# Kernel optimization log

Hardware: AMD Instinct MI355X
Metric: run time of the kernel (lower is better)

## Reference

```python
import jax, jax.numpy as jnp
import numpy as np

H = 768          # low-res grid side
S = 3            # scale_factor -> output is (H*S, H*S)
HID = 32         # hidden_channels
N = H * H


def _grid_edges(h):
    """8-neighbor directed edge list, same as create_graph's python loop."""
    idx = np.arange(h * h, dtype=np.int32).reshape(h, h)
    srcs, dsts = [], []
    for di in (-1, 0, 1):
        for dj in (-1, 0, 1):
            if di == 0 and dj == 0:
                continue
            rs = slice(max(0, -di), h - max(0, di))
            cs = slice(max(0, -dj), h - max(0, dj))
            rd = slice(max(0, di), h - max(0, -di))
            cd = slice(max(0, dj), h - max(0, -dj))
            srcs.append(idx[rs, cs].ravel())
            dsts.append(idx[rd, cd].ravel())
    return np.stack([np.concatenate(srcs), np.concatenate(dsts)])


def setup_inputs() -> dict:
    key = jax.random.key(0)
    ks = jax.random.split(key, 4)
    edge_index = jnp.asarray(_grid_edges(H))  # [2, E] int32
    x = jax.random.normal(ks[0], (N, 3), dtype=jnp.float32)
    W1 = jax.random.normal(ks[1], (3, HID), dtype=jnp.float32) * (1.0 / np.sqrt(3))
    W2 = jax.random.normal(ks[2], (HID, HID), dtype=jnp.float32) * (1.0 / np.sqrt(HID))
    W3 = jax.random.normal(ks[3], (HID, S * S), dtype=jnp.float32) * (1.0 / np.sqrt(HID))
    return {
        "x": x, "edge_index": edge_index,
        "W1": W1, "b1": jnp.zeros((HID,), jnp.float32),
        "W2": W2, "b2": jnp.zeros((HID,), jnp.float32),
        "W3": W3, "b3": jnp.zeros((S * S,), jnp.float32),
    }


def _gcn_layer(h, W, b, src, dst, norm_e, self_norm, n):
    # GCNConv: x' = D^-1/2 (A + I) D^-1/2 (x W) + b
    h = h @ W
    msg = h[src] * norm_e[:, None]                        # gather + normalize
    agg = jax.ops.segment_sum(msg, dst, num_segments=n)    # scatter-add
    return agg + h * self_norm[:, None] + b                # self-loop + bias


def reference(x, edge_index, W1, b1, W2, b2, W3, b3):
    n = x.shape[0]
    src, dst = edge_index[0], edge_index[1]
    # degrees with self-loops (PyG gcn_norm: deg on target col, +1 self loop)
    deg = jax.ops.segment_sum(jnp.ones(src.shape, jnp.float32), dst, num_segments=n) + 1.0
    dinv = jax.lax.rsqrt(deg)
    norm_e = dinv[src] * dinv[dst]
    self_norm = dinv * dinv

    h = jax.nn.relu(_gcn_layer(x, W1, b1, src, dst, norm_e, self_norm, n))
    h = jax.nn.relu(_gcn_layer(h, W2, b2, src, dst, norm_e, self_norm, n))
    h = _gcn_layer(h, W3, b3, src, dst, norm_e, self_norm, n)

    # pixel-shuffle reshape: [N, S*S] -> [1, H*S, H*S]
    out = h.reshape(1, H, H, S, S).transpose(0, 1, 3, 2, 4).reshape(1, H * S, H * S)
    return out
```

## Files before the change

### kernel.cpp

```cpp
#include <hip/hip_runtime.h>


constexpr int HH = 768, SS = 3;
constexpr int TI = 12, TJ = 24;
constexpr int NBJ = 32;
constexpr int NT = 512;

constexpr int G0C = 30;  constexpr int N0  = 540;
constexpr int S0C = 28;  constexpr int NS0 = 448;
constexpr int R3C = 26;  constexpr int NS1 = 364;
constexpr int NS1P = 368;
constexpr int ON  = 288;

constexpr int G1O = 0;
constexpr int D3O = 7168;
constexpr int SMEMF = 7536;

constexpr int TB0 = 0;
constexpr int TB1 = 1472;
constexpr int TB2 = 2944;
constexpr int OUT0 = 3328;
constexpr int OUT1 = 4480;
constexpr int OUT2 = 5632;

#define SWZ(row) ((((row) >> 1) & 3) << 2)

typedef _Float16 f16x8 __attribute__((ext_vector_type(8)));
typedef float    f32x4 __attribute__((ext_vector_type(4)));
using h2 = decltype(__builtin_amdgcn_cvt_pkrtz(0.f, 0.f));

#define PK(a, b)  __builtin_amdgcn_cvt_pkrtz((a), (b))
#define BC2(u)    __builtin_bit_cast(h2, (u))
#define BCU(x)    __builtin_bit_cast(uint32_t, (x))
#define MFMA16(a, b, c) __builtin_amdgcn_mfma_f32_16x16x32_f16((a), (b), (c), 0, 0, 0)

__device__ __forceinline__ float dinv_of(int gi, int gj) {
    int e = (1 + (gi > 0) + (gi < HH - 1)) * (1 + (gj > 0) + (gj < HH - 1));
    return e == 9 ? 0.33333334f : (e == 6 ? 0.40824829f : 0.5f);
}
__device__ __forceinline__ void add4(float4& a, const float4 v) {
    a.x += v.x; a.y += v.y; a.z += v.z; a.w += v.w;
}
#define FMA4G(acc, s, wp) { const float4 _w = *(const float4*)(wp); \
    acc.x += (s) * _w.x; acc.y += (s) * _w.y; acc.z += (s) * _w.z; acc.w += (s) * _w.w; }

__global__ __launch_bounds__(NT, 8) void gnn_fused(
    const float* __restrict__ x,
    const float* __restrict__ W1, const float* __restrict__ b1,
    const float* __restrict__ W2, const float* __restrict__ b2,
    const float* __restrict__ W3, const float* __restrict__ b3,
    float* __restrict__ out)
{
    __shared__ __align__(16) float smem[SMEMF];
    const int tid = threadIdx.x;
    const int lane = tid & 63, wid = tid >> 6;
    const int lr = lane & 15, lg = lane >> 4;
    const int bi = blockIdx.x / NBJ;
    const int bj = blockIdx.x % NBJ;
    const int oi = bi * TI, oj = bj * TJ;

    for (int n = tid; n < N0; n += NT) {
        int li = n / G0C, lj = n - li * G0C;
        int gi = oi - 3 + li, gj = oj - 3 + lj;
        float4 v = {0.f, 0.f, 0.f, 0.f};
        if ((unsigned)gi < HH && (unsigned)gj < HH) {
            float d = dinv_of(gi, gj);
            const float* xp = x + 3 * ((size_t)gi * HH + gj);
            v.x = d * xp[0]; v.y = d * xp[1]; v.z = d * xp[2];
        }
        *(float4*)&smem[G1O + n * 4] = v;
    }
    if (tid < NS1P) {
        float v = 0.f;
        if (tid < NS1) {
            int li = tid / R3C, lj = tid - li * R3C;
            int gi = oi - 1 + li, gj = oj - 1 + lj;
            if ((unsigned)gi < HH && (unsigned)gj < HH) v = dinv_of(gi, gj);
        }
        smem[D3O + tid] = v;
    }
    __syncthreads();

    float4 s0a = {0,0,0,0};
    float d2a = 0.f;
    if (tid < NS0) {
        int li = tid / S0C, lj = tid - li * S0C;
        int base = li * G0C + lj;
        #pragma unroll
        for (int di = 0; di < 3; ++di)
            #pragma unroll
            for (int dj = 0; dj < 3; ++dj)
                add4(s0a, *(const float4*)&smem[G1O + (base + di * G0C + dj) * 4]);
        int gi = oi - 2 + li, gj = oj - 2 + lj;
        if ((unsigned)gi < HH && (unsigned)gj < HH) d2a = dinv_of(gi, gj);
    }
    const int nA0 = wid * 16 + lr;
    const int nA1 = (wid + 8) * 16 + lr;
    const int nA2 = (wid + 16) * 16 + lr;
    const int fb0 = (nA0 / R3C) * S0C + (nA0 % R3C);
    const int fb1 = (nA1 / R3C) * S0C + (nA1 % R3C);
    const int fb2 = (nA2 / R3C) * S0C + (nA2 % R3C);
    __syncthreads();

    uint4 uw20, uw21, uw3;
    {
        const int k0 = 8 * lg;
        uw20.x = BCU(PK(W2[(k0+0)*32 + lr],      W2[(k0+1)*32 + lr]));
        uw20.y = BCU(PK(W2[(k0+2)*32 + lr],      W2[(k0+3)*32 + lr]));
        uw20.z = BCU(PK(W2[(k0+4)*32 + lr],      W2[(k0+5)*32 + lr]));
        uw20.w = BCU(PK(W2[(k0+6)*32 + lr],      W2[(k0+7)*32 + lr]));
        uw21.x = BCU(PK(W2[(k0+0)*32 + 16 + lr], W2[(k0+1)*32 + 16 + lr]));
        uw21.y = BCU(PK(W2[(k0+2)*32 + 16 + lr], W2[(k0+3)*32 + 16 + lr]));
        uw21.z = BCU(PK(W2[(k0+4)*32 + 16 + lr], W2[(k0+5)*32 + 16 + lr]));
        uw21.w = BCU(PK(W2[(k0+6)*32 + 16 + lr], W2[(k0+7)*32 + 16 + lr]));
        float a0w=0.f,b0w=0.f,a1w=0.f,b1w=0.f,a2w=0.f,b2w=0.f,a3w=0.f,b3w=0.f;
        if (lr < 9) {
            a0w = W3[(k0+0)*9 + lr]; b0w = W3[(k0+1)*9 + lr];
            a1w = W3[(k0+2)*9 + lr]; b1w = W3[(k0+3)*9 + lr];
            a2w = W3[(k0+4)*9 + lr]; b2w = W3[(k0+5)*9 + lr];
            a3w = W3[(k0+6)*9 + lr]; b3w = W3[(k0+7)*9 + lr];
        }
        uw3.x = BCU(PK(a0w, b0w)); uw3.y = BCU(PK(a1w, b1w));
        uw3.z = BCU(PK(a2w, b2w)); uw3.w = BCU(PK(a3w, b3w));
    }
    const float b2c0 = b2[lr], b2c1 = b2[16 + lr];

    if (tid < NS0) {
        uint32_t g[16];
        #pragma unroll
        for (int q = 0; q < 8; ++q) {
            float4 a = {0,0,0,0};
            FMA4G(a, s0a.x, W1 + 4 * q)
            FMA4G(a, s0a.y, W1 + 32 + 4 * q)
            FMA4G(a, s0a.z, W1 + 64 + 4 * q)
            const float4 bb = *(const float4*)&b1[4 * q];
            float gx = d2a * fmaxf(d2a * a.x + bb.x, 0.f);
            float gy = d2a * fmaxf(d2a * a.y + bb.y, 0.f);
            float gz = d2a * fmaxf(d2a * a.z + bb.z, 0.f);
            float gw = d2a * fmaxf(d2a * a.w + bb.w, 0.f);
            g[2 * q]     = BCU(PK(gx, gy));
            g[2 * q + 1] = BCU(PK(gz, gw));
        }
        const int sz = SWZ(tid);
        uint4 u;
        u.x = g[0];  u.y = g[1];  u.z = g[2];  u.w = g[3];
        *(uint4*)&smem[G1O + tid * 16 + (0 ^ sz)] = u;
        u.x = g[4];  u.y = g[5];  u.z = g[6];  u.w = g[7];
        *(uint4*)&smem[G1O + tid * 16 + (4 ^ sz)] = u;
        u.x = g[8];  u.y = g[9];  u.z = g[10]; u.w = g[11];
        *(uint4*)&smem[G1O + tid * 16 + (8 ^ sz)] = u;
        u.x = g[12]; u.y = g[13]; u.z = g[14]; u.w = g[15];
        *(uint4*)&smem[G1O + tid * 16 + (12 ^ sz)] = u;
    }
    __syncthreads();

    const f16x8 bw20 = __builtin_bit_cast(f16x8, uw20);
    const f16x8 bw21 = __builtin_bit_cast(f16x8, uw21);
    const f16x8 bw3  = __builtin_bit_cast(f16x8, uw3);

    #define TAP(rr) (*(const uint4*)&smem[G1O + (rr) * 16 + ((4 * lg) ^ SWZ(rr))])
    #define ROWSUM(rr, o0, o1, o2) { \
        const uint4 va = TAP((rr)+(o0)); const uint4 vb = TAP((rr)+(o1)); const uint4 vc = TAP((rr)+(o2)); \
        r0 = (BC2(va.x) + BC2(vb.x)) + BC2(vc.x); \
        r1 = (BC2(va.y) + BC2(vb.y)) + BC2(vc.y); \
        r2 = (BC2(va.z) + BC2(vb.z)) + BC2(vc.z); \
        r3 = (BC2(va.w) + BC2(vb.w)) + BC2(vc.w); }

    #define BS2MM2(fb, cc0, cc1) { \
        h2 r0, r1, r2, r3, s0_, s1_, s2_, s3_; \
        ROWSUM((fb), 0, 1, 2)               s0_ = r0; s1_ = r1; s2_ = r2; s3_ = r3; \
        ROWSUM((fb) + S0C, 0, 1, 2)         s0_ += r0; s1_ += r1; s2_ += r2; s3_ += r3; \
        ROWSUM((fb) + 2 * S0C, 0, 1, 2)     s0_ += r0; s1_ += r1; s2_ += r2; s3_ += r3; \
        uint4 af_; af_.x = BCU(s0_); af_.y = BCU(s1_); af_.z = BCU(s2_); af_.w = BCU(s3_); \
        const f16x8 aa_ = __builtin_bit_cast(f16x8, af_); \
        cc0 = MFMA16(aa_, bw20, cc0); \
        cc1 = MFMA16(aa_, bw21, cc1); }

    f32x4 c00 = {0,0,0,0}, c01 = {0,0,0,0};
    f32x4 c10 = {0,0,0,0}, c11 = {0,0,0,0};
    f32x4 c20 = {0,0,0,0}, c21 = {0,0,0,0};
    BS2MM2(fb0, c00, c01)
    BS2MM2(fb1, c10, c11)
    if (wid < 7) { BS2MM2(fb2, c20, c21) }
    __syncthreads();

    _Float16* hp = (_Float16*)smem;
    #define WRH(rt, cc0, cc1) { \
        const int nb = (rt) * 16 + lg * 4; \
        const float4 dd = *(const float4*)&smem[D3O + nb]; \
        _Pragma("unroll") \
        for (int r = 0; r < 4; ++r) { \
            const float dv = r == 0 ? dd.x : (r == 1 ? dd.y : (r == 2 ? dd.z : dd.w)); \
            const float h0 = dv * fmaxf(dv * cc0[r] + b2c0, 0.f); \
            const float h1 = dv * fmaxf(dv * cc1[r] + b2c1, 0.f); \
            const int row_ = nb + r; \
            const int sz_ = SWZ(row_); \
            hp[2 * (G1O + row_ * 16 + (((lr >> 1)) ^ sz_)) + (lr & 1)] = (_Float16)h0; \
            hp[2 * (G1O + row_ * 16 + ((8 + (lr >> 1)) ^ sz_)) + (lr & 1)] = (_Float16)h1; } }

    WRH(wid, c00, c01)
    WRH(wid + 8, c10, c11)
    if (wid < 7) { WRH(wid + 16, c20, c21) }
    __syncthreads();

    #define AFRAG(rt) __builtin_bit_cast(f16x8, \
        *(const uint4*)&smem[G1O + ((rt) * 16 + lr) * 16 + ((4 * lg) ^ SWZ((rt) * 16 + lr))])
    f16x8 a30 = AFRAG(wid);
    f16x8 a31 = AFRAG(wid + 8);
    f16x8 a32 = a30;
    if (wid < 7) a32 = AFRAG(wid + 16);
    __syncthreads();

    #define MM3TILE(rt, af) { \
        f32x4 tt = {0.f, 0.f, 0.f, 0.f}; \
        tt = MFMA16((af), bw3, tt); \
        const int nb = (rt) * 16 + lg * 4; \
        if (lr < 4) { \
            smem[TB0 + (nb + 0) * 4 + lr] = tt[0]; \
            smem[TB0 + (nb + 1) * 4 + lr] = tt[1]; \
            smem[TB0 + (nb + 2) * 4 + lr] = tt[2]; \
            smem[TB0 + (nb + 3) * 4 + lr] = tt[3]; \
        } else if (lr < 8) { \
            smem[TB1 + (nb + 0) * 4 + lr - 4] = tt[0]; \
            smem[TB1 + (nb + 1) * 4 + lr - 4] = tt[1]; \
            smem[TB1 + (nb + 2) * 4 + lr - 4] = tt[2]; \
            smem[TB1 + (nb + 3) * 4 + lr - 4] = tt[3]; \
        } else if (lr == 8) { \
            smem[TB2 + nb + 0] = tt[0]; \
            smem[TB2 + nb + 1] = tt[1]; \
            smem[TB2 + nb + 2] = tt[2]; \
            smem[TB2 + nb + 3] = tt[3]; } }

    MM3TILE(wid, a30)
    MM3TILE(wid + 8, a31)
    if (wid < 7) { MM3TILE(wid + 16, a32) }
    __syncthreads();

    for (int item = tid; item < 3 * ON; item += NT) {
        int p = item / ON, n = item - p * ON;
        int li = n / TJ, lj = n - li * TJ;
        int src = li * R3C + lj;
        float d = dinv_of(oi + li, oj + lj);
        if (p == 2) {
            float s = 0.f;
            #pragma unroll
            for (int di = 0; di < 3; ++di)
                #pragma unroll
                for (int dj = 0; dj < 3; ++dj)
                    s += smem[TB2 + src + di * R3C + dj];
            smem[OUT2 + n] = d * s + b3[8];
        } else {
            const int tb = p ? TB1 : TB0;
            float4 s = {0.f, 0.f, 0.f, 0.f};
            #pragma unroll
            for (int di = 0; di < 3; ++di)
                #pragma unroll
                for (int dj = 0; dj < 3; ++dj)
                    add4(s, *(const float4*)&smem[tb + (src + di * R3C + dj) * 4]);
            const float4 bb = *(const float4*)&b3[4 * p];
            float4 o;
            o.x = d * s.x + bb.x; o.y = d * s.y + bb.y;
            o.z = d * s.z + bb.z; o.w = d * s.w + bb.w;
            *(float4*)&smem[(p ? OUT1 : OUT0) + n * 4] = o;
        }
    }
    __syncthreads();

    #define ORD(n, c) ((c) < 8 ? smem[((c) < 4 ? OUT0 : OUT1) + (n) * 4 + ((c) & 3)] \
                               : smem[OUT2 + (n)])
    for (int q = tid; q < 36 * 18; q += NT) {
        int rr = q / 18, cc0 = 4 * (q % 18);
        int ii = rr / 3, si = rr - 3 * ii;
        float4 o;
        { int cc = cc0 + 0, jj = cc / 3, sj = cc - 3 * jj; o.x = ORD(ii * TJ + jj, si * 3 + sj); }
        { int cc = cc0 + 1, jj = cc / 3, sj = cc - 3 * jj; o.y = ORD(ii * TJ + jj, si * 3 + sj); }
        { int cc = cc0 + 2, jj = cc / 3, sj = cc - 3 * jj; o.z = ORD(ii * TJ + jj, si * 3 + sj); }
        { int cc = cc0 + 3, jj = cc / 3, sj = cc - 3 * jj; o.w = ORD(ii * TJ + jj, si * 3 + sj); }
        *(float4*)&out[(size_t)(oi * SS + rr) * (HH * SS) + oj * SS + cc0] = o;
    }
}

extern "C" void kernel_launch(void* const* d_in, const int* in_sizes, int n_in,
                              void* d_out, int out_size, void* d_ws, size_t ws_size,
                              hipStream_t stream) {
    const float* x  = (const float*)d_in[0];
    const float* W1 = (const float*)d_in[2];
    const float* b1 = (const float*)d_in[3];
    const float* W2 = (const float*)d_in[4];
    const float* b2 = (const float*)d_in[5];
    const float* W3 = (const float*)d_in[6];
    const float* b3 = (const float*)d_in[7];
    float* out = (float*)d_out;

    gnn_fused<<<dim3(64 * NBJ), dim3(NT), 0, stream>>>(x, W1, b1, W2, b2, W3, b3, out);
}
```

Baseline: 38.38 us.

## Aggregate layer-3 inputs before the W3 MFMA and fuse the normalization epilogue

```diff
diff --git a/kernel.cpp b/kernel.cpp
--- a/kernel.cpp
+++ b/kernel.cpp
@@ -14,16 +14,13 @@
 
 constexpr int G1O = 0;
 constexpr int D3O = 7168;
-constexpr int SMEMF = 7536;
-
-constexpr int TB0 = 0;
-constexpr int TB1 = 1472;
-constexpr int TB2 = 2944;
-constexpr int OUT0 = 3328;
-constexpr int OUT1 = 4480;
-constexpr int OUT2 = 5632;
+constexpr int OUT0 = 7536;
+constexpr int OUT1 = 8688;
+constexpr int OUT2 = 9840;
+constexpr int SMEMF = 10128;
 
 #define SWZ(row) ((((row) >> 1) & 3) << 2)
+#define DIV24(n) (((n) * 683) >> 14)
 
 typedef _Float16 f16x8 __attribute__((ext_vector_type(8)));
 typedef float    f32x4 __attribute__((ext_vector_type(4)));
@@ -124,6 +121,7 @@
         uw3.z = BCU(PK(a2w, b2w)); uw3.w = BCU(PK(a3w, b3w));
     }
     const float b2c0 = b2[lr], b2c1 = b2[16 + lr];
+    const float b3c  = (lr < 9) ? b3[lr] : 0.f;
 
     if (tid < NS0) {
         uint32_t g[16];
@@ -203,67 +201,33 @@
     if (wid < 7) { WRH(wid + 16, c20, c21) }
     __syncthreads();
 
-    #define AFRAG(rt) __builtin_bit_cast(f16x8, \
-        *(const uint4*)&smem[G1O + ((rt) * 16 + lr) * 16 + ((4 * lg) ^ SWZ((rt) * 16 + lr))])
-    f16x8 a30 = AFRAG(wid);
-    f16x8 a31 = AFRAG(wid + 8);
-    f16x8 a32 = a30;
-    if (wid < 7) a32 = AFRAG(wid + 16);
-    __syncthreads();
-
-    #define MM3TILE(rt, af) { \
-        f32x4 tt = {0.f, 0.f, 0.f, 0.f}; \
-        tt = MFMA16((af), bw3, tt); \
-        const int nb = (rt) * 16 + lg * 4; \
-        if (lr < 4) { \
-            smem[TB0 + (nb + 0) * 4 + lr] = tt[0]; \
-            smem[TB0 + (nb + 1) * 4 + lr] = tt[1]; \
-            smem[TB0 + (nb + 2) * 4 + lr] = tt[2]; \
-            smem[TB0 + (nb + 3) * 4 + lr] = tt[3]; \
-        } else if (lr < 8) { \
-            smem[TB1 + (nb + 0) * 4 + lr - 4] = tt[0]; \
-            smem[TB1 + (nb + 1) * 4 + lr - 4] = tt[1]; \
-            smem[TB1 + (nb + 2) * 4 + lr - 4] = tt[2]; \
-            smem[TB1 + (nb + 3) * 4 + lr - 4] = tt[3]; \
-        } else if (lr == 8) { \
-            smem[TB2 + nb + 0] = tt[0]; \
-            smem[TB2 + nb + 1] = tt[1]; \
-            smem[TB2 + nb + 2] = tt[2]; \
-            smem[TB2 + nb + 3] = tt[3]; } }
-
-    MM3TILE(wid, a30)
-    MM3TILE(wid + 8, a31)
-    if (wid < 7) { MM3TILE(wid + 16, a32) }
-    __syncthreads();
-
-    for (int item = tid; item < 3 * ON; item += NT) {
-        int p = item / ON, n = item - p * ON;
-        int li = n / TJ, lj = n - li * TJ;
-        int src = li * R3C + lj;
-        float d = dinv_of(oi + li, oj + lj);
-        if (p == 2) {
-            float s = 0.f;
-            #pragma unroll
-            for (int di = 0; di < 3; ++di)
-                #pragma unroll
-                for (int dj = 0; dj < 3; ++dj)
-                    s += smem[TB2 + src + di * R3C + dj];
-            smem[OUT2 + n] = d * s + b3[8];
-        } else {
-            const int tb = p ? TB1 : TB0;
-            float4 s = {0.f, 0.f, 0.f, 0.f};
-            #pragma unroll
-            for (int di = 0; di < 3; ++di)
-                #pragma unroll
-                for (int dj = 0; dj < 3; ++dj)
-                    add4(s, *(const float4*)&smem[tb + (src + di * R3C + dj) * 4]);
-            const float4 bb = *(const float4*)&b3[4 * p];
-            float4 o;
-            o.x = d * s.x + bb.x; o.y = d * s.y + bb.y;
-            o.z = d * s.z + bb.z; o.w = d * s.w + bb.w;
-            *(float4*)&smem[(p ? OUT1 : OUT0) + n * 4] = o;
-        }
-    }
+    #define BS3MM3(ot) { \
+        const int nOl = (ot) * 16 + lr; \
+        const int liO = DIV24(nOl); \
+        const int hb = nOl + 2 * liO;           \
+        h2 r0, r1, r2, r3, s0_, s1_, s2_, s3_; \
+        ROWSUM(hb, 0, 1, 2)                 s0_ = r0; s1_ = r1; s2_ = r2; s3_ = r3; \
+        ROWSUM(hb + R3C, 0, 1, 2)           s0_ += r0; s1_ += r1; s2_ += r2; s3_ += r3; \
+        ROWSUM(hb + 2 * R3C, 0, 1, 2)       s0_ += r0; s1_ += r1; s2_ += r2; s3_ += r3; \
+        uint4 af_; af_.x = BCU(s0_); af_.y = BCU(s1_); af_.z = BCU(s2_); af_.w = BCU(s3_); \
+        f32x4 tt = {0,0,0,0}; \
+        tt = MFMA16(__builtin_bit_cast(f16x8, af_), bw3, tt); \
+        const int nb = (ot) * 16 + lg * 4; \
+        if (lr < 9) { \
+            _Pragma("unroll") \
+            for (int r = 0; r < 4; ++r) { \
+                const int node = nb + r; \
+                const int liN = DIV24(node); \
+                const float d = smem[D3O + node + 2 * liN + 27]; \
+                const float o = d * tt[r] + b3c; \
+                if (lr < 4)      smem[OUT0 + node * 4 + lr] = o; \
+                else if (lr < 8) smem[OUT1 + node * 4 + lr - 4] = o; \
+                else             smem[OUT2 + node] = o; \
+            } } }
+
+    BS3MM3(wid)
+    BS3MM3(wid + 8)
+    if (wid < 2) { BS3MM3(wid + 16) }
     __syncthreads();
 
     #define ORD(n, c) ((c) < 8 ? smem[((c) < 4 ? OUT0 : OUT1) + (n) * 4 + ((c) & 3)] \
```

Result: slower. 40.56 us (+5.7%).
